# Kernel tuning notes

Measured on AMD Instinct MI355X. Metric: run time of the kernel, lower is better.

## Reference

```python
import jax, jax.numpy as jnp
import numpy as np

N, E, G = 50000, 800000, 64          # nodes, edges, graphs in batch
F, HG, HL = 64, 128, 128             # node feat, graph hidden, lin hidden
AVG_LOG = float(np.log(9.0))         # from deg histogram [0]*8+[1]: log(8+1)


def setup_inputs() -> dict:
    key = jax.random.key(0)
    ks = jax.random.split(key, 24)
    def w(k, shape):
        return 0.1 * jax.random.normal(k, shape, jnp.float32)
    return {
        "x": jax.random.normal(ks[0], (N, F), jnp.float32),
        "edge_index": jax.random.randint(ks[1], (2, E), 0, N),
        "edge_attr": jax.random.normal(ks[2], (E, 1), jnp.float32),
        "batch": jnp.sort(jax.random.randint(ks[3], (N,), 0, G)),
        # PNAConv params (towers=1, pre_layers=1, post_layers=1, edge_dim=1)
        "W_edge": w(ks[4], (1, F)),      "b_edge": w(ks[5], (F,)),
        "W_pre": w(ks[6], (3 * F, F)),   "b_pre": w(ks[7], (F,)),
        "W_post": w(ks[8], (13 * F, HG)), "b_post": w(ks[9], (HG,)),
        "W_lin": w(ks[10], (HG, HG)),    "b_lin": w(ks[11], (HG,)),
        # bn1 / fc2 / bn2
        "g1": jnp.ones((HG,)), "be1": jnp.zeros((HG,)),
        "W2": w(ks[12], (HG, HL)), "b2": w(ks[13], (HL,)),
        "g2": jnp.ones((HL,)), "be2": jnp.zeros((HL,)),
        # one resnet block: fc/bn/fc/bn
        "Wr1": w(ks[14], (HL, HL)), "br1": w(ks[15], (HL,)),
        "gr1": jnp.ones((HL,)), "ber1": jnp.zeros((HL,)),
        "Wr2": w(ks[16], (HL, HL)), "br2": w(ks[17], (HL,)),
        "gr2": jnp.ones((HL,)), "ber2": jnp.zeros((HL,)),
        "W_out": w(ks[18], (HL, 1)), "b_out": w(ks[19], (1,)),
    }


def _bn(z, g, b):
    # BatchNorm1d, training mode: biased batch stats, eps=1e-5
    mu = z.mean(0)
    var = ((z - mu) ** 2).mean(0)
    return (z - mu) * jax.lax.rsqrt(var + 1e-5) * g + b


def _pna(x, edge_index, edge_attr, W_edge, b_edge, W_pre, b_pre,
         W_post, b_post, W_lin, b_lin):
    src, dst = edge_index[0], edge_index[1]  # messages flow j->i, aggregate at dst
    e = edge_attr @ W_edge + b_edge                               # [E, F]
    m = jnp.concatenate([x[dst], x[src], e], -1) @ W_pre + b_pre  # [E, F]
    ones_e = jnp.ones((m.shape[0],), m.dtype)
    cnt = jax.ops.segment_sum(ones_e, dst, N)                     # in-degree
    cnt1 = jnp.maximum(cnt, 1.0)
    mean = jax.ops.segment_sum(m, dst, N) / cnt1[:, None]
    mean2 = jax.ops.segment_sum(m * m, dst, N) / cnt1[:, None]
    std = jnp.sqrt(jax.nn.relu(mean2 - mean * mean) + 1e-5)
    has = (cnt > 0)[:, None]
    mn = jnp.where(has, jax.ops.segment_min(m, dst, N), 0.0)
    mx = jnp.where(has, jax.ops.segment_max(m, dst, N), 0.0)
    agg = jnp.concatenate([mean, mn, mx, std], -1)                # [N, 4F]
    amp = (jnp.log(cnt1 + 1.0) / AVG_LOG)[:, None]                # amplification scaler
    out = jnp.concatenate([agg, agg * amp, agg / amp], -1)        # [N, 12F]
    out = jnp.concatenate([x, out], -1) @ W_post + b_post         # [N, HG]
    return out @ W_lin + b_lin                                    # [N, HG]


def reference(x, edge_index, edge_attr, batch,
              W_edge, b_edge, W_pre, b_pre, W_post, b_post, W_lin, b_lin,
              g1, be1, W2, b2, g2, be2,
              Wr1, br1, gr1, ber1, Wr2, br2, gr2, ber2,
              W_out, b_out):
    h = _pna(x, edge_index, edge_attr, W_edge, b_edge, W_pre, b_pre,
             W_post, b_post, W_lin, b_lin)
    # global_mean_pool over graphs
    gc = jnp.maximum(jax.ops.segment_sum(jnp.ones((h.shape[0],), h.dtype), batch, G), 1.0)
    z = jax.ops.segment_sum(h, batch, G) / gc[:, None]            # [G, HG]
    z = jax.nn.relu(_bn(z, g1, be1))
    z = jax.nn.relu(_bn(z @ W2 + b2, g2, be2))
    r = z
    z = jax.nn.relu(_bn(z @ Wr1 + br1, gr1, ber1))
    z = jax.nn.relu(_bn(z @ Wr2 + br2, gr2, ber2) + r)
    return z @ W_out + b_out                                      # [G, 1]
```

## Files before the change

### kernel.cpp

```cpp
#include <hip/hip_runtime.h>
#include <hip/hip_bf16.h>

using bf16 = __hip_bfloat16;

#define F 64
#define HG 128
#define HL 128
#define AVG_LOG_INV 0.45511961331341866f
#define BSH 5
#define BNODES 32
#define BCAP 1024
#define BTILE 8192
#define NBMAX 1664
#define NBTMAX 128

typedef short short8 __attribute__((ext_vector_type(8)));
typedef float floatx4 __attribute__((ext_vector_type(4)));

__device__ __forceinline__ float b2f(bf16 v) { return __bfloat162float(v); }
__device__ __forceinline__ bf16 f2b(float v) { return __float2bfloat16(v); }
__device__ __forceinline__ short f2bs(float v) { bf16 h = f2b(v); return *(short*)&h; }

__device__ __forceinline__ unsigned packbf2(float x, float y) {
    bf16 a = f2b(x), b = f2b(y);
    unsigned short ua = *(unsigned short*)&a, ub = *(unsigned short*)&b;
    return ((unsigned)ub << 16) | (unsigned)ua;
}

__device__ __forceinline__ float wave_sum(float v) {
    #pragma unroll
    for (int m = 32; m > 0; m >>= 1) v += __shfl_xor(v, m);
    return v;
}

__global__ __launch_bounds__(512) void k_prep(
    const float* __restrict__ x, const float* __restrict__ W_pre,
    bf16* __restrict__ AB, int N,
    const int* __restrict__ ei, const float* __restrict__ ea,
    int* __restrict__ ofs, int2* __restrict__ gout, int E,
    float* __restrict__ gfeat, int* __restrict__ gcnt,
    int NB, int GF, int G, int NBT,
    const float* __restrict__ W_edge, const float* __restrict__ b_edge,
    const float* __restrict__ b_pre, float* __restrict__ uc) {
    __shared__ __align__(16) char smem[18432];
    int t = threadIdx.x;
    int gtid = blockIdx.x * 512 + t;
    int gstr = gridDim.x * 512;
    for (int i = gtid; i < GF; i += gstr) gfeat[i] = 0.f;
    for (int i = gtid; i < G; i += gstr) gcnt[i] = 0;

    if (blockIdx.x < NBT) {
        int* hist = (int*)smem;
        int* aux  = hist + NBMAX;
        int p = blockIdx.x;
        for (int i = t; i < NB; i += 512) hist[i] = 0;
        __syncthreads();
        int base = p * BTILE;
        int lim = E - base; if (lim > BTILE) lim = BTILE;
        int nq = lim >> 2;
        const int4* dst4 = (const int4*)(ei + E + base);
        for (int q = t; q < nq; q += 512) {
            int4 d = dst4[q];
            atomicAdd(&hist[d.x >> BSH], 1);
            atomicAdd(&hist[d.y >> BSH], 1);
            atomicAdd(&hist[d.z >> BSH], 1);
            atomicAdd(&hist[d.w >> BSH], 1);
        }
        for (int i = (nq << 2) + t; i < lim; i += 512)
            atomicAdd(&hist[ei[E + base + i] >> BSH], 1);
        __syncthreads();
        int b0 = t * 4;
        int c0 = 0, c1 = 0, c2 = 0, c3 = 0;
        if (b0 < NB)     c0 = hist[b0];
        if (b0 + 1 < NB) c1 = hist[b0 + 1];
        if (b0 + 2 < NB) c2 = hist[b0 + 2];
        if (b0 + 3 < NB) c3 = hist[b0 + 3];
        int tot = c0 + c1 + c2 + c3;
        aux[t] = tot;
        __syncthreads();
        for (int d = 1; d < 512; d <<= 1) {
            int v = (t >= d) ? aux[t - d] : 0;
            __syncthreads();
            aux[t] += v;
            __syncthreads();
        }
        int run = aux[t] - tot;
        __syncthreads();
        size_t orow = (size_t)p * (NB + 1);
        if (b0 < NB)     { hist[b0]     = run; ofs[orow + b0]     = run; run += c0; }
        if (b0 + 1 < NB) { hist[b0 + 1] = run; ofs[orow + b0 + 1] = run; run += c1; }
        if (b0 + 2 < NB) { hist[b0 + 2] = run; ofs[orow + b0 + 2] = run; run += c2; }
        if (b0 + 3 < NB) { hist[b0 + 3] = run; ofs[orow + b0 + 3] = run; run += c3; }
        if (t == 0) ofs[orow + NB] = lim;
        for (int i = t; i < NB; i += 512) aux[i] = 0;
        __syncthreads();
        const int4* src4 = (const int4*)(ei + base);
        const float4* ea4 = (const float4*)(ea + base);
        int2* seg = gout + (size_t)p * BTILE;
        for (int q = t; q < nq; q += 512) {
            int4 s = src4[q], d = dst4[q];
            float4 v = ea4[q];
            int bb, pos;
            bb = d.x >> BSH; pos = hist[bb] + atomicAdd(&aux[bb], 1);
            seg[pos] = make_int2((d.x << 16) | s.x, __float_as_int(v.x));
            bb = d.y >> BSH; pos = hist[bb] + atomicAdd(&aux[bb], 1);
            seg[pos] = make_int2((d.y << 16) | s.y, __float_as_int(v.y));
            bb = d.z >> BSH; pos = hist[bb] + atomicAdd(&aux[bb], 1);
            seg[pos] = make_int2((d.z << 16) | s.z, __float_as_int(v.z));
            bb = d.w >> BSH; pos = hist[bb] + atomicAdd(&aux[bb], 1);
            seg[pos] = make_int2((d.w << 16) | s.w, __float_as_int(v.w));
        }
        for (int i = (nq << 2) + t; i < lim; i += 512) {
            int s = ei[base + i], d = ei[E + base + i];
            int bb = d >> BSH;
            int pos = hist[bb] + atomicAdd(&aux[bb], 1);
            seg[pos] = make_int2((d << 16) | s, __float_as_int(ea[base + i]));
        }
    } else {
        if (blockIdx.x == NBT && t < 64) {
            int f = t;
            float u = 0.f, c = b_pre[f];
            for (int k = 0; k < 64; k++) {
                float w3 = W_pre[(128 + k) * 64 + f];
                u += W_edge[k] * w3;
                c += b_edge[k] * w3;
            }
            uc[f] = u; uc[64 + f] = c;
        }
        unsigned short* wt = (unsigned short*)smem;
        for (int idx = t; idx < 8192; idx += 512) {
            int k = idx >> 7, m = idx & 127;
            float v = W_pre[((m & 64) + k) * 64 + (m & 63)];
            wt[m * 72 + k] = (unsigned short)f2bs(v);
        }
        __syncthreads();

        int lane = t & 63;
        int row = lane & 15, quad = lane >> 4;
        int w = (blockIdx.x - NBT) * 8 + (t >> 6);
        int nwaves = (gridDim.x - NBT) * 8;
        int ntiles = (N + 15) >> 4;

        for (int tile = w; tile < ntiles; tile += nwaves) {
            int m0 = tile << 4;
            int node_a = m0 + row; if (node_a >= N) node_a = N - 1;
            short8 a[2];
            #pragma unroll
            for (int h = 0; h < 2; h++) {
                const float* xp = x + (size_t)node_a * 64 + h * 32 + quad * 8;
                floatx4 v0 = *(const floatx4*)xp;
                floatx4 v1 = *(const floatx4*)(xp + 4);
                #pragma unroll
                for (int j = 0; j < 4; j++) { a[h][j] = f2bs(v0[j]); a[h][4 + j] = f2bs(v1[j]); }
            }
            #pragma unroll
            for (int tt = 0; tt < 8; tt++) {
                int fbase = tt * 16;
                floatx4 c = {0.f, 0.f, 0.f, 0.f};
                #pragma unroll
                for (int h = 0; h < 2; h++) {
                    short8 bfr = *(const short8*)(wt + (fbase + row) * 72 + h * 32 + quad * 8);
                    c = __builtin_amdgcn_mfma_f32_16x16x32_bf16(a[h], bfr, c, 0, 0, 0);
                }
                #pragma unroll
                for (int r = 0; r < 4; r++) {
                    int node = m0 + quad * 4 + r;
                    if (node < N) AB[(size_t)node * 128 + fbase + row] = f2b(c[r]);
                }
            }
        }
    }
}

__global__ __launch_bounds__(512) void k_edge(
    const bf16* __restrict__ AB, const int2* __restrict__ gout,
    const int* __restrict__ ofs, const float* __restrict__ uc,
    const int* __restrict__ batch, const float* __restrict__ x,
    float* __restrict__ gfeat, int* __restrict__ gcnt,
    int N, int NB, int NBT) {
    __shared__ int2 recs[BCAP], sortd[BCAP];
    __shared__ int ncnt[BNODES], nofs[BNODES], nrank[BNODES];
    __shared__ int gid[BNODES];
    __shared__ unsigned lstat[BNODES][128];
    __shared__ float lamp[BNODES], liamp[BNODES];
    __shared__ int runlo[NBTMAX], runlen[NBTMAX], runpre[NBTMAX];
    __shared__ int etot_s;
    int t = threadIdx.x;
    int b = blockIdx.x;
    int nn = N - b * BNODES; if (nn > BNODES) nn = BNODES;

    if (t < NBTMAX) { runlo[t] = 0; runlen[t] = 0; }
    if (t < BNODES) {
        ncnt[t] = 0; nrank[t] = 0;
        if (t < nn) gid[t] = batch[b * BNODES + t];
    }
    __syncthreads();
    if (t < NBT) {
        int lo = ofs[(size_t)t * (NB + 1) + b];
        int hi = ofs[(size_t)t * (NB + 1) + b + 1];
        runlo[t] = lo; runlen[t] = hi - lo;
    }
    __syncthreads();
    if (t < NBTMAX) runpre[t] = runlen[t];
    __syncthreads();
    for (int d = 1; d < NBTMAX; d <<= 1) {
        int v = 0;
        if (t < NBTMAX && t >= d) v = runpre[t - d];
        __syncthreads();
        if (t < NBTMAX) runpre[t] += v;
        __syncthreads();
    }
    if (t == NBTMAX - 1) etot_s = runpre[NBTMAX - 1];
    int ex = 0;
    if (t < NBTMAX) ex = runpre[t] - runlen[t];
    __syncthreads();
    if (t < NBTMAX) runpre[t] = ex;
    __syncthreads();
    int ecnt = etot_s; if (ecnt > BCAP) ecnt = BCAP;
    for (int i = t; i < ecnt; i += 512) {
        int lo2 = 0, hi2 = NBT;
        while (hi2 - lo2 > 1) {
            int mid = (lo2 + hi2) >> 1;
            if (runpre[mid] <= i) lo2 = mid; else hi2 = mid;
        }
        recs[i] = gout[(size_t)lo2 * BTILE + runlo[lo2] + (i - runpre[lo2])];
    }
    __syncthreads();
    for (int i = t; i < ecnt; i += 512)
        atomicAdd(&ncnt[((unsigned)recs[i].x >> 16) & (BNODES - 1)], 1);
    __syncthreads();
    if (t < BNODES) {
        int v = ncnt[t], inc = v;
        #pragma unroll
        for (int m = 1; m < BNODES; m <<= 1) { int u = __shfl_up(inc, m); if (t >= m) inc += u; }
        nofs[t] = inc - v;
    }
    __syncthreads();
    for (int i = t; i < ecnt; i += 512) {
        int2 r = recs[i];
        int nl = ((unsigned)r.x >> 16) & (BNODES - 1);
        int k = atomicAdd(&nrank[nl], 1);
        sortd[nofs[nl] + k] = r;
    }
    __syncthreads();

    int lane = t & 63, w = t >> 6;
    int half = lane & 31, hi32 = lane >> 5;
    float2 u2 = *(const float2*)(uc + 2 * half);
    float2 c2 = *(const float2*)(uc + 64 + 2 * half);

    for (int nl = w; nl < nn; nl += 8) {
        int n = b * BNODES + nl;
        int lo = nofs[nl], cnt = ncnt[nl], hi = lo + cnt;

        unsigned apack = *(const unsigned*)(AB + (size_t)n * 128 + 2 * half);
        float acx = __uint_as_float(apack << 16) + c2.x;
        float acy = __uint_as_float(apack & 0xffff0000u) + c2.y;

        float sx = 0.f, sy = 0.f, qx = 0.f, qy = 0.f;
        float mnx = 3.4e38f, mny = 3.4e38f, mxx = -3.4e38f, mxy = -3.4e38f;

        auto acc2 = [&](unsigned bp, float eav) {
            float bx = __uint_as_float(bp << 16);
            float by = __uint_as_float(bp & 0xffff0000u);
            float m0 = fmaf(eav, u2.x, acx) + bx;
            float m1 = fmaf(eav, u2.y, acy) + by;
            sx += m0; qx = fmaf(m0, m0, qx);
            sy += m1; qy = fmaf(m1, m1, qy);
            mnx = fminf(mnx, m0); mxx = fmaxf(mxx, m0);
            mny = fminf(mny, m1); mxy = fmaxf(mxy, m1);
        };
        auto gaddr = [&](int sn) {
            return (const unsigned*)(AB + (size_t)sn * 128 + 64 + 2 * half);
        };

        for (int base = lo; base < hi; base += 64) {
            int nb = hi - base; if (nb > 64) nb = 64;
            int2 rec = (lane < nb) ? sortd[base + lane] : make_int2(0, 0);
            int vsn = rec.x & 0xFFFF;
            float vea = __int_as_float(rec.y);
            int i = 0;
            for (; i + 8 <= nb; i += 8) {
                int sn0 = __shfl(vsn, i + hi32);
                int sn1 = __shfl(vsn, i + 2 + hi32);
                int sn2 = __shfl(vsn, i + 4 + hi32);
                int sn3 = __shfl(vsn, i + 6 + hi32);
                float e0 = __shfl(vea, i + hi32);
                float e1 = __shfl(vea, i + 2 + hi32);
                float e2 = __shfl(vea, i + 4 + hi32);
                float e3 = __shfl(vea, i + 6 + hi32);
                unsigned b0 = *gaddr(sn0);
                unsigned b1 = *gaddr(sn1);
                unsigned b2 = *gaddr(sn2);
                unsigned b3 = *gaddr(sn3);
                acc2(b0, e0); acc2(b1, e1); acc2(b2, e2); acc2(b3, e3);
            }
            for (; i + 2 <= nb; i += 2) {
                int   sn = __shfl(vsn, i + hi32);
                float ev = __shfl(vea, i + hi32);
                acc2(*gaddr(sn), ev);
            }
            if (i < nb) {
                int   sn = __shfl(vsn, i);
                float ev = __shfl(vea, i);
                unsigned bp = *gaddr(sn);
                if (hi32 == 0) acc2(bp, ev);
            }
        }
        sx += __shfl_xor(sx, 32); sy += __shfl_xor(sy, 32);
        qx += __shfl_xor(qx, 32); qy += __shfl_xor(qy, 32);
        mnx = fminf(mnx, __shfl_xor(mnx, 32)); mny = fminf(mny, __shfl_xor(mny, 32));
        mxx = fmaxf(mxx, __shfl_xor(mxx, 32)); mxy = fmaxf(mxy, __shfl_xor(mxy, 32));

        float c1 = (cnt > 0) ? (float)cnt : 1.f;
        float inv = 1.f / c1;
        float mex = sx * inv, mey = sy * inv;
        float vx = qx * inv - mex * mex; if (vx < 0.f) vx = 0.f;
        float vy = qy * inv - mey * mey; if (vy < 0.f) vy = 0.f;
        float sdx = sqrtf(vx + 1e-5f), sdy = sqrtf(vy + 1e-5f);
        if (cnt == 0) { mnx = mny = mxx = mxy = 0.f; }

        if (hi32 == 0) {
            lstat[nl][half]      = packbf2(mex, mey);
            lstat[nl][32 + half] = packbf2(mnx, mny);
        } else {
            lstat[nl][64 + half] = packbf2(mxx, mxy);
            lstat[nl][96 + half] = packbf2(sdx, sdy);
        }
        if (lane == 0) {
            float amp = logf(c1 + 1.f) * AVG_LOG_INV;
            lamp[nl] = amp; liamp[nl] = 1.f / amp;
        }
    }
    __syncthreads();

    if (t < 128) {
        int c = t;
        int elem = ((c >> 5) << 6) + ((c & 31) << 1);
        float s1x = 0.f, s1y = 0.f, s2x = 0.f, s2y = 0.f, s3x = 0.f, s3y = 0.f;
        float sxv = 0.f;
        int cnt = 0;
        int cur = gid[0];
        for (int nl = 0; nl < nn; nl++) {
            int g = gid[nl];
            if (g != cur) {
                float* gf = gfeat + (size_t)cur * 832;
                unsafeAtomicAdd(&gf[64 + elem], s1x);
                unsafeAtomicAdd(&gf[65 + elem], s1y);
                unsafeAtomicAdd(&gf[320 + elem], s2x);
                unsafeAtomicAdd(&gf[321 + elem], s2y);
                unsafeAtomicAdd(&gf[576 + elem], s3x);
                unsafeAtomicAdd(&gf[577 + elem], s3y);
                if (t < 64) unsafeAtomicAdd(&gf[t], sxv);
                if (t == 0) atomicAdd(&gcnt[cur], cnt);
                s1x = s1y = s2x = s2y = s3x = s3y = 0.f; sxv = 0.f; cnt = 0;
                cur = g;
            }
            unsigned p = lstat[nl][c];
            float bx = __uint_as_float(p << 16);
            float by = __uint_as_float(p & 0xffff0000u);
            float a = lamp[nl], ia = liamp[nl];
            s1x += bx; s2x = fmaf(bx, a, s2x); s3x = fmaf(bx, ia, s3x);
            s1y += by; s2y = fmaf(by, a, s2y); s3y = fmaf(by, ia, s3y);
            if (t < 64) sxv += x[(size_t)(b * BNODES + nl) * 64 + t];
            cnt++;
        }
        float* gf = gfeat + (size_t)cur * 832;
        unsafeAtomicAdd(&gf[64 + elem], s1x);
        unsafeAtomicAdd(&gf[65 + elem], s1y);
        unsafeAtomicAdd(&gf[320 + elem], s2x);
        unsafeAtomicAdd(&gf[321 + elem], s2y);
        unsafeAtomicAdd(&gf[576 + elem], s3x);
        unsafeAtomicAdd(&gf[577 + elem], s3y);
        if (t < 64) unsafeAtomicAdd(&gf[t], sxv);
        if (t == 0) atomicAdd(&gcnt[cur], cnt);
    }
}

__global__ void k_post1(const float* __restrict__ gfeat, const int* __restrict__ gcnt,
                        const float* __restrict__ W_post, const float* __restrict__ b_post,
                        const float* __restrict__ W_lin, const float* __restrict__ b_lin,
                        float* __restrict__ Zin) {
    int g = blockIdx.x, t = threadIdx.x;
    int j = t & 127, h = t >> 7;
    __shared__ float feat[832];
    __shared__ float part[256];
    __shared__ float z1[128];
    int cg = gcnt[g];
    float r = 1.f / ((cg > 0) ? (float)cg : 1.f);
    for (int i = t; i < 832; i += 256) feat[i] = gfeat[(size_t)g * 832 + i] * r;
    __syncthreads();
    float acc = (h == 0) ? b_post[j] : 0.f;
    const float* Wp = W_post + (size_t)(h * 416) * 128 + j;
    const float* fp = feat + h * 416;
    #pragma unroll 8
    for (int k = 0; k < 416; k++) acc += fp[k] * Wp[(size_t)k * 128];
    part[t] = acc;
    __syncthreads();
    if (t < 128) z1[j] = part[j] + part[128 + j];
    __syncthreads();
    float a2 = (h == 0) ? b_lin[j] : 0.f;
    #pragma unroll
    for (int k = 0; k < 64; k++) a2 += z1[h * 64 + k] * W_lin[(h * 64 + k) * 128 + j];
    part[t] = a2;
    __syncthreads();
    if (t < 128) {
        float v = part[j] + part[128 + j];
        if (cg == 0) v = 0.f;
        Zin[g * 128 + j] = v;
    }
}

__global__ void k_mlpcol(const float* __restrict__ in, const float* __restrict__ W,
                         const float* __restrict__ bias,
                         const float* __restrict__ gamma, const float* __restrict__ beta,
                         const float* __restrict__ res,
                         const float* __restrict__ g_in, const float* __restrict__ be_in,
                         float* __restrict__ outp) {
    __shared__ float A[64 * 129];
    __shared__ float part[4 * 64];
    int t = threadIdx.x;
    int j = blockIdx.x;

    for (int i = t; i < 8192; i += 256) A[(i >> 7) * 129 + (i & 127)] = in[i];
    __syncthreads();

    if (g_in) {
        if (t < 128) {
            int c = t;
            float mu = 0.f;
            for (int r = 0; r < 64; r++) mu += A[r * 129 + c];
            mu *= (1.f / 64.f);
            float var = 0.f;
            for (int r = 0; r < 64; r++) { float d = A[r * 129 + c] - mu; var += d * d; }
            var *= (1.f / 64.f);
            float sc = rsqrtf(var + 1e-5f) * g_in[c], sh = be_in[c];
            for (int r = 0; r < 64; r++) {
                float v = (A[r * 129 + c] - mu) * sc + sh;
                A[r * 129 + c] = v > 0.f ? v : 0.f;
            }
        }
        __syncthreads();
    }

    int r = t & 63, q = t >> 6;
    float acc = 0.f;
    int k0 = q * 32;
    #pragma unroll
    for (int k = 0; k < 32; k++) acc += A[r * 129 + k0 + k] * W[(k0 + k) * 128 + j];
    part[q * 64 + r] = acc;
    __syncthreads();

    if (t < 64) {
        float v = part[t] + part[64 + t] + part[128 + t] + part[192 + t] + bias[j];
        float mu = wave_sum(v) * (1.f / 64.f);
        float d = v - mu;
        float var = wave_sum(d * d) * (1.f / 64.f);
        float o = d * rsqrtf(var + 1e-5f) * gamma[j] + beta[j];
        if (res) o += res[t * 128 + j];
        outp[t * 128 + j] = o > 0.f ? o : 0.f;
    }
}

__global__ void k_out(const float* __restrict__ z4, const float* __restrict__ W_out,
                      const float* b_out, float* __restrict__ out) {
    int g = threadIdx.x;
    float acc = b_out[0];
    for (int j = 0; j < 128; j++) acc += z4[g * 128 + j] * W_out[j];
    out[g] = acc;
}

extern "C" void kernel_launch(void* const* d_in, const int* in_sizes, int n_in,
                              void* d_out, int out_size, void* d_ws, size_t ws_size,
                              hipStream_t stream) {
    const float* x      = (const float*)d_in[0];
    const int*   ei     = (const int*)d_in[1];
    const float* ea     = (const float*)d_in[2];
    const int*   batch  = (const int*)d_in[3];
    const float* W_edge = (const float*)d_in[4];
    const float* b_edge = (const float*)d_in[5];
    const float* W_pre  = (const float*)d_in[6];
    const float* b_pre  = (const float*)d_in[7];
    const float* W_post = (const float*)d_in[8];
    const float* b_post = (const float*)d_in[9];
    const float* W_lin  = (const float*)d_in[10];
    const float* b_lin  = (const float*)d_in[11];
    const float* g1     = (const float*)d_in[12];
    const float* be1    = (const float*)d_in[13];
    const float* W2     = (const float*)d_in[14];
    const float* b2     = (const float*)d_in[15];
    const float* g2     = (const float*)d_in[16];
    const float* be2    = (const float*)d_in[17];
    const float* Wr1    = (const float*)d_in[18];
    const float* br1    = (const float*)d_in[19];
    const float* gr1    = (const float*)d_in[20];
    const float* ber1   = (const float*)d_in[21];
    const float* Wr2    = (const float*)d_in[22];
    const float* br2    = (const float*)d_in[23];
    const float* gr2    = (const float*)d_in[24];
    const float* ber2   = (const float*)d_in[25];
    const float* W_out  = (const float*)d_in[26];
    const float* b_out  = (const float*)d_in[27];
    float* out = (float*)d_out;

    const int N = in_sizes[0] / F;
    const int E = in_sizes[1] / 2;
    const int G = out_size;
    const int NB = (N + BNODES - 1) >> BSH;

    char* p = (char*)d_ws;
    auto alloc = [&](size_t nbytes) { void* r = p; p += (nbytes + 255) & ~(size_t)255; return r; };
    const int NBT = (E + BTILE - 1) / BTILE;
    bf16*  AB     = (bf16*)alloc((size_t)N * 128 * sizeof(bf16));
    int2*  gout   = (int2*)alloc((size_t)NBT * BTILE * sizeof(int2));
    int*   ofs    = (int*)alloc((size_t)NBT * (NB + 1) * sizeof(int));
    float* uc     = (float*)alloc(128 * sizeof(float));
    float* gfeat  = (float*)alloc((size_t)G * 832 * sizeof(float));
    int*   gcnt   = (int*)alloc((size_t)G * sizeof(int));
    float* Zin    = (float*)alloc(64 * 128 * sizeof(float));
    float* z2b    = (float*)alloc(64 * 128 * sizeof(float));
    float* z3b    = (float*)alloc(64 * 128 * sizeof(float));
    float* z4b    = (float*)alloc(64 * 128 * sizeof(float));

    const int GF = G * 832;
    const int NAB = (((N + 15) >> 4) + 7) >> 3;

    k_prep<<<NBT + NAB, 512, 0, stream>>>(x, W_pre, AB, N, ei, ea, ofs, gout, E,
                                          gfeat, gcnt, NB, GF, G, NBT,
                                          W_edge, b_edge, b_pre, uc);
    k_edge<<<NB, 512, 0, stream>>>(AB, gout, ofs, uc, batch, x, gfeat, gcnt, N, NB, NBT);
    k_post1<<<G, 256, 0, stream>>>(gfeat, gcnt, W_post, b_post, W_lin, b_lin, Zin);
    k_mlpcol<<<HG, 256, 0, stream>>>(Zin, W2, b2, g2, be2, nullptr, g1, be1, z2b);
    k_mlpcol<<<HL, 256, 0, stream>>>(z2b, Wr1, br1, gr1, ber1, nullptr, nullptr, nullptr, z3b);
    k_mlpcol<<<HL, 256, 0, stream>>>(z3b, Wr2, br2, gr2, ber2, z2b, nullptr, nullptr, z4b);
    k_out<<<1, 64, 0, stream>>>(z4b, W_out, b_out, out);
}
```

Baseline: 227.0 us.

## Process two nodes per wave in k_edge and replace block scan with wave scan

The per-node gather loop now handles two destination nodes per wavefront at once. It issues four source-row loads for each node before accumulating, which puts more gathers in flight, and it reads edge records straight from LDS instead of shuffling them. The block-wide run-offset prefix scan is replaced by a single-wave shuffle scan, removing several __syncthreads, and the degree counting is folded into the record gather loop. The x-sum and graph-count accumulation move to separate thread groups so they run alongside the stat reduction. A launch_bounds occupancy hint of 8 is added, which may limit registers and cause spills given the doubled accumulator state.

Result: no change. 223.1 us (-1.7%).

```diff
diff --git a/kernel.cpp b/kernel.cpp
--- a/kernel.cpp
+++ b/kernel.cpp
@@ -172,7 +172,7 @@
     }
 }
 
-__global__ __launch_bounds__(512) void k_edge(
+__global__ __launch_bounds__(512, 8) void k_edge(
     const bf16* __restrict__ AB, const int2* __restrict__ gout,
     const int* __restrict__ ofs, const float* __restrict__ uc,
     const int* __restrict__ batch, const float* __restrict__ x,
@@ -183,51 +183,49 @@
     __shared__ int gid[BNODES];
     __shared__ unsigned lstat[BNODES][128];
     __shared__ float lamp[BNODES], liamp[BNODES];
-    __shared__ int runlo[NBTMAX], runlen[NBTMAX], runpre[NBTMAX];
+    __shared__ int runlo[NBTMAX], runpre[NBTMAX];
     __shared__ int etot_s;
     int t = threadIdx.x;
     int b = blockIdx.x;
     int nn = N - b * BNODES; if (nn > BNODES) nn = BNODES;
 
-    if (t < NBTMAX) { runlo[t] = 0; runlen[t] = 0; }
-    if (t < BNODES) {
-        ncnt[t] = 0; nrank[t] = 0;
-        if (t < nn) gid[t] = batch[b * BNODES + t];
-    }
-    __syncthreads();
-    if (t < NBT) {
-        int lo = ofs[(size_t)t * (NB + 1) + b];
-        int hi = ofs[(size_t)t * (NB + 1) + b + 1];
-        runlo[t] = lo; runlen[t] = hi - lo;
-    }
-    __syncthreads();
-    if (t < NBTMAX) runpre[t] = runlen[t];
-    __syncthreads();
-    for (int d = 1; d < NBTMAX; d <<= 1) {
-        int v = 0;
-        if (t < NBTMAX && t >= d) v = runpre[t - d];
-        __syncthreads();
-        if (t < NBTMAX) runpre[t] += v;
-        __syncthreads();
-    }
-    if (t == NBTMAX - 1) etot_s = runpre[NBTMAX - 1];
-    int ex = 0;
-    if (t < NBTMAX) ex = runpre[t] - runlen[t];
-    __syncthreads();
-    if (t < NBTMAX) runpre[t] = ex;
-    __syncthreads();
+    if (t < 64) {
+        int l = t;
+        int p0 = 2 * l, p1 = 2 * l + 1;
+        int lo0 = 0, len0 = 0, lo1 = 0, len1 = 0;
+        if (p0 < NBT) {
+            lo0 = ofs[(size_t)p0 * (NB + 1) + b];
+            len0 = ofs[(size_t)p0 * (NB + 1) + b + 1] - lo0;
+        }
+        if (p1 < NBT) {
+            lo1 = ofs[(size_t)p1 * (NB + 1) + b];
+            len1 = ofs[(size_t)p1 * (NB + 1) + b + 1] - lo1;
+        }
+        runlo[p0] = lo0; runlo[p1] = lo1;
+        int s = len0 + len1, inc = s;
+        #pragma unroll
+        for (int m = 1; m < 64; m <<= 1) { int u = __shfl_up(inc, m); if (l >= m) inc += u; }
+        int ex = inc - s;
+        runpre[p0] = ex; runpre[p1] = ex + len0;
+        if (l == 63) etot_s = inc;
+    } else if (t < 96) {
+        int i = t - 64;
+        ncnt[i] = 0; nrank[i] = 0;
+        if (i < nn) gid[i] = batch[b * BNODES + i];
+    }
+    __syncthreads();
+
     int ecnt = etot_s; if (ecnt > BCAP) ecnt = BCAP;
     for (int i = t; i < ecnt; i += 512) {
-        int lo2 = 0, hi2 = NBT;
+        int lo2 = 0, hi2 = NBTMAX;
         while (hi2 - lo2 > 1) {
             int mid = (lo2 + hi2) >> 1;
             if (runpre[mid] <= i) lo2 = mid; else hi2 = mid;
         }
-        recs[i] = gout[(size_t)lo2 * BTILE + runlo[lo2] + (i - runpre[lo2])];
-    }
-    __syncthreads();
-    for (int i = t; i < ecnt; i += 512)
-        atomicAdd(&ncnt[((unsigned)recs[i].x >> 16) & (BNODES - 1)], 1);
+        int2 r = gout[(size_t)lo2 * BTILE + runlo[lo2] + (i - runpre[lo2])];
+        recs[i] = r;
+        atomicAdd(&ncnt[((unsigned)r.x >> 16) & (BNODES - 1)], 1);
+    }
     __syncthreads();
     if (t < BNODES) {
         int v = ncnt[t], inc = v;
@@ -249,88 +247,103 @@
     float2 u2 = *(const float2*)(uc + 2 * half);
     float2 c2 = *(const float2*)(uc + 64 + 2 * half);
 
-    for (int nl = w; nl < nn; nl += 8) {
-        int n = b * BNODES + nl;
-        int lo = nofs[nl], cnt = ncnt[nl], hi = lo + cnt;
-
-        unsigned apack = *(const unsigned*)(AB + (size_t)n * 128 + 2 * half);
-        float acx = __uint_as_float(apack << 16) + c2.x;
-        float acy = __uint_as_float(apack & 0xffff0000u) + c2.y;
-
-        float sx = 0.f, sy = 0.f, qx = 0.f, qy = 0.f;
-        float mnx = 3.4e38f, mny = 3.4e38f, mxx = -3.4e38f, mxy = -3.4e38f;
-
-        auto acc2 = [&](unsigned bp, float eav) {
-            float bx = __uint_as_float(bp << 16);
-            float by = __uint_as_float(bp & 0xffff0000u);
-            float m0 = fmaf(eav, u2.x, acx) + bx;
-            float m1 = fmaf(eav, u2.y, acy) + by;
-            sx += m0; qx = fmaf(m0, m0, qx);
-            sy += m1; qy = fmaf(m1, m1, qy);
-            mnx = fminf(mnx, m0); mxx = fmaxf(mxx, m0);
-            mny = fminf(mny, m1); mxy = fmaxf(mxy, m1);
-        };
+    for (int nl = w; nl < nn; nl += 16) {
+        int nlA = nl, nlB = nl + 8;
+        bool hasB = (nlB < nn);
+        int nA = b * BNODES + nlA;
+        int nB = b * BNODES + (hasB ? nlB : nlA);
+        int loA = nofs[nlA], cntA = ncnt[nlA];
+        int loB = hasB ? nofs[nlB] : 0, cntB = hasB ? ncnt[nlB] : 0;
+
+        unsigned apA = *(const unsigned*)(AB + (size_t)nA * 128 + 2 * half);
+        unsigned apB = *(const unsigned*)(AB + (size_t)nB * 128 + 2 * half);
+        float acxA = __uint_as_float(apA << 16) + c2.x;
+        float acyA = __uint_as_float(apA & 0xffff0000u) + c2.y;
+        float acxB = __uint_as_float(apB << 16) + c2.x;
+        float acyB = __uint_as_float(apB & 0xffff0000u) + c2.y;
+
+        float sxA = 0.f, syA = 0.f, qxA = 0.f, qyA = 0.f;
+        float mnxA = 3.4e38f, mnyA = 3.4e38f, mxxA = -3.4e38f, mxyA = -3.4e38f;
+        float sxB = 0.f, syB = 0.f, qxB = 0.f, qyB = 0.f;
+        float mnxB = 3.4e38f, mnyB = 3.4e38f, mxxB = -3.4e38f, mxyB = -3.4e38f;
+
         auto gaddr = [&](int sn) {
             return (const unsigned*)(AB + (size_t)sn * 128 + 64 + 2 * half);
         };
 
-        for (int base = lo; base < hi; base += 64) {
-            int nb = hi - base; if (nb > 64) nb = 64;
-            int2 rec = (lane < nb) ? sortd[base + lane] : make_int2(0, 0);
-            int vsn = rec.x & 0xFFFF;
-            float vea = __int_as_float(rec.y);
-            int i = 0;
-            for (; i + 8 <= nb; i += 8) {
-                int sn0 = __shfl(vsn, i + hi32);
-                int sn1 = __shfl(vsn, i + 2 + hi32);
-                int sn2 = __shfl(vsn, i + 4 + hi32);
-                int sn3 = __shfl(vsn, i + 6 + hi32);
-                float e0 = __shfl(vea, i + hi32);
-                float e1 = __shfl(vea, i + 2 + hi32);
-                float e2 = __shfl(vea, i + 4 + hi32);
-                float e3 = __shfl(vea, i + 6 + hi32);
-                unsigned b0 = *gaddr(sn0);
-                unsigned b1 = *gaddr(sn1);
-                unsigned b2 = *gaddr(sn2);
-                unsigned b3 = *gaddr(sn3);
-                acc2(b0, e0); acc2(b1, e1); acc2(b2, e2); acc2(b3, e3);
-            }
-            for (; i + 2 <= nb; i += 2) {
-                int   sn = __shfl(vsn, i + hi32);
-                float ev = __shfl(vea, i + hi32);
-                acc2(*gaddr(sn), ev);
-            }
-            if (i < nb) {
-                int   sn = __shfl(vsn, i);
-                float ev = __shfl(vea, i);
-                unsigned bp = *gaddr(sn);
-                if (hi32 == 0) acc2(bp, ev);
-            }
-        }
-        sx += __shfl_xor(sx, 32); sy += __shfl_xor(sy, 32);
-        qx += __shfl_xor(qx, 32); qy += __shfl_xor(qy, 32);
-        mnx = fminf(mnx, __shfl_xor(mnx, 32)); mny = fminf(mny, __shfl_xor(mny, 32));
-        mxx = fmaxf(mxx, __shfl_xor(mxx, 32)); mxy = fmaxf(mxy, __shfl_xor(mxy, 32));
-
-        float c1 = (cnt > 0) ? (float)cnt : 1.f;
-        float inv = 1.f / c1;
-        float mex = sx * inv, mey = sy * inv;
-        float vx = qx * inv - mex * mex; if (vx < 0.f) vx = 0.f;
-        float vy = qy * inv - mey * mey; if (vy < 0.f) vy = 0.f;
-        float sdx = sqrtf(vx + 1e-5f), sdy = sqrtf(vy + 1e-5f);
-        if (cnt == 0) { mnx = mny = mxx = mxy = 0.f; }
-
-        if (hi32 == 0) {
-            lstat[nl][half]      = packbf2(mex, mey);
-            lstat[nl][32 + half] = packbf2(mnx, mny);
-        } else {
-            lstat[nl][64 + half] = packbf2(mxx, mxy);
-            lstat[nl][96 + half] = packbf2(sdx, sdy);
-        }
-        if (lane == 0) {
-            float amp = logf(c1 + 1.f) * AVG_LOG_INV;
-            lamp[nl] = amp; liamp[nl] = 1.f / amp;
-        }
+        for (int i = hi32; (i < cntA) || (i < cntB); i += 8) {
+            unsigned bpA[4], bpB[4];
+            #pragma unroll
+            for (int j = 0; j < 4; j++) {
+                int idx = i + 2 * j;
+                int e = loA + (idx < cntA ? idx : 0);
+                bpA[j] = *gaddr(sortd[e].x & 0xFFFF);
+            }
+            #pragma unroll
+            for (int j = 0; j < 4; j++) {
+                int idx = i + 2 * j;
+                int e = loB + (idx < cntB ? idx : 0);
+                bpB[j] = *gaddr(sortd[e].x & 0xFFFF);
+            }
+            #pragma unroll
+            for (int j = 0; j < 4; j++) {
+                int idx = i + 2 * j;
+                if (idx < cntA) {
+                    float eav = __int_as_float(sortd[loA + idx].y);
+                    float bx = __uint_as_float(bpA[j] << 16);
+                    float by = __uint_as_float(bpA[j] & 0xffff0000u);
+                    float m0 = fmaf(eav, u2.x, acxA) + bx;
+                    float m1 = fmaf(eav, u2.y, acyA) + by;
+                    sxA += m0; qxA = fmaf(m0, m0, qxA);
+                    syA += m1; qyA = fmaf(m1, m1, qyA);
+                    mnxA = fminf(mnxA, m0); mxxA = fmaxf(mxxA, m0);
+                    mnyA = fminf(mnyA, m1); mxyA = fmaxf(mxyA, m1);
+                }
+            }
+            #pragma unroll
+            for (int j = 0; j < 4; j++) {
+                int idx = i + 2 * j;
+                if (idx < cntB) {
+                    float eav = __int_as_float(sortd[loB + idx].y);
+                    float bx = __uint_as_float(bpB[j] << 16);
+                    float by = __uint_as_float(bpB[j] & 0xffff0000u);
+                    float m0 = fmaf(eav, u2.x, acxB) + bx;
+                    float m1 = fmaf(eav, u2.y, acyB) + by;
+                    sxB += m0; qxB = fmaf(m0, m0, qxB);
+                    syB += m1; qyB = fmaf(m1, m1, qyB);
+                    mnxB = fminf(mnxB, m0); mxxB = fmaxf(mxxB, m0);
+                    mnyB = fminf(mnyB, m1); mxyB = fmaxf(mxyB, m1);
+                }
+            }
+        }
+
+        auto finish = [&](int nl_, int cnt, float sx, float sy, float qx, float qy,
+                          float mnx, float mny, float mxx, float mxy) {
+            sx += __shfl_xor(sx, 32); sy += __shfl_xor(sy, 32);
+            qx += __shfl_xor(qx, 32); qy += __shfl_xor(qy, 32);
+            mnx = fminf(mnx, __shfl_xor(mnx, 32)); mny = fminf(mny, __shfl_xor(mny, 32));
+            mxx = fmaxf(mxx, __shfl_xor(mxx, 32)); mxy = fmaxf(mxy, __shfl_xor(mxy, 32));
+            float c1 = (cnt > 0) ? (float)cnt : 1.f;
+            float inv = 1.f / c1;
+            float mex = sx * inv, mey = sy * inv;
+            float vx = qx * inv - mex * mex; if (vx < 0.f) vx = 0.f;
+            float vy = qy * inv - mey * mey; if (vy < 0.f) vy = 0.f;
+            float sdx = sqrtf(vx + 1e-5f), sdy = sqrtf(vy + 1e-5f);
+            if (cnt == 0) { mnx = mny = mxx = mxy = 0.f; }
+            if (hi32 == 0) {
+                lstat[nl_][half]      = packbf2(mex, mey);
+                lstat[nl_][32 + half] = packbf2(mnx, mny);
+            } else {
+                lstat[nl_][64 + half] = packbf2(mxx, mxy);
+                lstat[nl_][96 + half] = packbf2(sdx, sdy);
+            }
+            if (lane == 0) {
+                float amp = logf(c1 + 1.f) * AVG_LOG_INV;
+                lamp[nl_] = amp; liamp[nl_] = 1.f / amp;
+            }
+        };
+        finish(nlA, cntA, sxA, syA, qxA, qyA, mnxA, mnyA, mxxA, mxyA);
+        if (hasB) finish(nlB, cntB, sxB, syB, qxB, qyB, mnxB, mnyB, mxxB, mxyB);
     }
     __syncthreads();
 
@@ -338,8 +351,6 @@
         int c = t;
         int elem = ((c >> 5) << 6) + ((c & 31) << 1);
         float s1x = 0.f, s1y = 0.f, s2x = 0.f, s2y = 0.f, s3x = 0.f, s3y = 0.f;
-        float sxv = 0.f;
-        int cnt = 0;
         int cur = gid[0];
         for (int nl = 0; nl < nn; nl++) {
             int g = gid[nl];
@@ -351,9 +362,7 @@
                 unsafeAtomicAdd(&gf[321 + elem], s2y);
                 unsafeAtomicAdd(&gf[576 + elem], s3x);
                 unsafeAtomicAdd(&gf[577 + elem], s3y);
-                if (t < 64) unsafeAtomicAdd(&gf[t], sxv);
-                if (t == 0) atomicAdd(&gcnt[cur], cnt);
-                s1x = s1y = s2x = s2y = s3x = s3y = 0.f; sxv = 0.f; cnt = 0;
+                s1x = s1y = s2x = s2y = s3x = s3y = 0.f;
                 cur = g;
             }
             unsigned p = lstat[nl][c];
@@ -362,8 +371,6 @@
             float a = lamp[nl], ia = liamp[nl];
             s1x += bx; s2x = fmaf(bx, a, s2x); s3x = fmaf(bx, ia, s3x);
             s1y += by; s2y = fmaf(by, a, s2y); s3y = fmaf(by, ia, s3y);
-            if (t < 64) sxv += x[(size_t)(b * BNODES + nl) * 64 + t];
-            cnt++;
         }
         float* gf = gfeat + (size_t)cur * 832;
         unsafeAtomicAdd(&gf[64 + elem], s1x);
@@ -372,8 +379,27 @@
         unsafeAtomicAdd(&gf[321 + elem], s2y);
         unsafeAtomicAdd(&gf[576 + elem], s3x);
         unsafeAtomicAdd(&gf[577 + elem], s3y);
-        if (t < 64) unsafeAtomicAdd(&gf[t], sxv);
-        if (t == 0) atomicAdd(&gcnt[cur], cnt);
+    } else if (t < 192) {
+        int c = t - 128;
+        float sxv = 0.f;
+        int cur = gid[0];
+        for (int nl = 0; nl < nn; nl++) {
+            int g = gid[nl];
+            if (g != cur) {
+                unsafeAtomicAdd(&gfeat[(size_t)cur * 832 + c], sxv);
+                sxv = 0.f; cur = g;
+            }
+            sxv += x[(size_t)(b * BNODES + nl) * 64 + c];
+        }
+        unsafeAtomicAdd(&gfeat[(size_t)cur * 832 + c], sxv);
+    } else if (t == 192) {
+        int cnt = 0, cur = gid[0];
+        for (int nl = 0; nl < nn; nl++) {
+            int g = gid[nl];
+            if (g != cur) { atomicAdd(&gcnt[cur], cnt); cnt = 0; cur = g; }
+            cnt++;
+        }
+        atomicAdd(&gcnt[cur], cnt);
     }
 }
 
```
